# Kernel tuning notes

Hardware: AMD Instinct MI355X
Metric: run time of the kernel (lower is better)

## Reference

```python
import jax, jax.numpy as jnp
import numpy as np

N = 50000
E = 800000
HIDDEN = 128
NUM_HEADS = 8
D_HEAD = HIDDEN // NUM_HEADS


def setup_inputs() -> dict:
    key = jax.random.key(0)
    ks = jax.random.split(key, 12)
    sc = 1.0 / np.sqrt(HIDDEN)
    inp = {
        "h": jax.random.normal(ks[0], (N, HIDDEN), dtype=jnp.float32),
        "rows": jax.random.randint(ks[1], (E,), 0, N, dtype=jnp.int32),
        "cols": jax.random.randint(ks[2], (E,), 0, N, dtype=jnp.int32),
        "Wq": jax.random.normal(ks[3], (HIDDEN, HIDDEN), dtype=jnp.float32) * sc,
        "bq": jax.random.normal(ks[4], (HIDDEN,), dtype=jnp.float32) * sc,
        "Wk": jax.random.normal(ks[5], (HIDDEN, HIDDEN), dtype=jnp.float32) * sc,
        "bk": jax.random.normal(ks[6], (HIDDEN,), dtype=jnp.float32) * sc,
        "Wv": jax.random.normal(ks[7], (HIDDEN, HIDDEN), dtype=jnp.float32) * sc,
        "bv": jax.random.normal(ks[8], (HIDDEN,), dtype=jnp.float32) * sc,
        "Wo": jax.random.normal(ks[9], (HIDDEN, HIDDEN), dtype=jnp.float32) * sc,
        "bo": jax.random.normal(ks[10], (HIDDEN,), dtype=jnp.float32) * sc,
    }
    return inp


def reference(h, rows, cols, Wq, bq, Wk, bk, Wv, bv, Wo, bo):
    n = h.shape[0]
    scaling = D_HEAD ** (-0.5)
    # projections; torch-style reshape splits hidden as (d_head, num_heads)
    q = ((h @ Wq.T + bq).reshape(n, D_HEAD, NUM_HEADS)) * scaling
    k = (h @ Wk.T + bk).reshape(n, D_HEAD, NUM_HEADS)
    v = (h @ Wv.T + bv).reshape(n, D_HEAD, NUM_HEADS)
    # SDDMM: per-edge, per-head score = q[row] . k[col]   -> [E, H]
    scores = jnp.einsum("edh,edh->eh", q[rows], k[cols])
    # row-wise (destination) stable softmax over variable-degree neighborhoods
    m = jax.ops.segment_max(scores, rows, num_segments=n)  # [N, H]
    e = jnp.exp(scores - m[rows])
    s = jax.ops.segment_sum(e, rows, num_segments=n)  # [N, H]
    attn = e / s[rows]  # [E, H]
    # SpMM: out[i] = sum_{(i,j) in E} attn[e] * v[j]
    out = jax.ops.segment_sum(attn[:, None, :] * v[cols], rows, num_segments=n)
    return out.reshape(n, HIDDEN) @ Wo.T + bo
```

## Files before the change

### kernel.cpp

```cpp
#include <hip/hip_runtime.h>
#include <math.h>

#define N_NODES 50000
#define N_EDGES 800000
#define HID 128
#define CAP 64

#define SCAT_TH   (N_EDGES / 8)
#define SCAT_BLK  ((SCAT_TH + 255) / 256)
#define WCVT_BLK  64
#define HCVT_BLK  (N_NODES * HID / 4 / 256)
#define PREP_BLK  (SCAT_BLK + WCVT_BLK + HCVT_BLK)

#define QKV_BX    ((N_NODES + 31) / 32)
#define ATTN_BLK  ((N_NODES + 3) / 4)
#define OUT_BLK   ((N_NODES + 63) / 64)

typedef _Float16 f16_t;
typedef f16_t f16x8 __attribute__((ext_vector_type(8)));
typedef f16_t f16x2 __attribute__((ext_vector_type(2)));
typedef float f32x4 __attribute__((ext_vector_type(4)));

__device__ __forceinline__ ushort f2h_bits(float x) {
    union { f16_t h; ushort u; } c; c.h = (f16_t)x; return c.u;
}
__device__ __forceinline__ f16x2 as_h2(uint u) {
    union { uint u_; f16x2 h; } c; c.u_ = u; return c.h;
}

__global__ __launch_bounds__(256) void prep(
    const float* __restrict__ h,
    const float* __restrict__ Wq, const float* __restrict__ Wk,
    const float* __restrict__ Wv, const float* __restrict__ Wo,
    ushort* __restrict__ hf, ushort* __restrict__ wf,
    const int* __restrict__ rows, const int* __restrict__ cols,
    int* __restrict__ cnt, ushort* __restrict__ slots)
{
    const int b = blockIdx.x;
    const int tid = threadIdx.x;

    if (b < SCAT_BLK) {
        const int t = b * 256 + tid;
        if (t < SCAT_TH) {
            const int4* r4 = (const int4*)rows + (size_t)t * 2;
            const int4* c4 = (const int4*)cols + (size_t)t * 2;
            int4 ra = r4[0], rb2 = r4[1];
            int4 ca = c4[0], cb = c4[1];
            const int r[8] = {ra.x, ra.y, ra.z, ra.w, rb2.x, rb2.y, rb2.z, rb2.w};
            const int c[8] = {ca.x, ca.y, ca.z, ca.w, cb.x, cb.y, cb.z, cb.w};
            int p[8];
#pragma unroll
            for (int u = 0; u < 8; ++u)
                p[u] = atomicAdd(&cnt[r[u] << 4], 1);
#pragma unroll
            for (int u = 0; u < 8; ++u)
                if (p[u] < CAP) slots[(size_t)r[u] * CAP + p[u]] = (ushort)c[u];
        }
    } else if (b < SCAT_BLK + WCVT_BLK) {
        const int t = (b - SCAT_BLK) * 256 + tid;
        const int m = t >> 12, i = t & 4095;
        const float* src = (m == 0) ? Wq : (m == 1) ? Wk : (m == 2) ? Wv : Wo;
        float4 f = ((const float4*)src)[i];
        ushort4 o;
        o.x = f2h_bits(f.x); o.y = f2h_bits(f.y);
        o.z = f2h_bits(f.z); o.w = f2h_bits(f.w);
        ((ushort4*)(wf + m * 16384))[i] = o;
    } else {
        const int t = (b - SCAT_BLK - WCVT_BLK) * 256 + tid;
        float4 f = ((const float4*)h)[t];
        ushort4 o;
        o.x = f2h_bits(f.x); o.y = f2h_bits(f.y);
        o.z = f2h_bits(f.z); o.w = f2h_bits(f.w);
        ((ushort4*)hf)[t] = o;
    }
}

__global__ __launch_bounds__(256) void gemm_qkv(
    const ushort* __restrict__ hf, const ushort* __restrict__ wf,
    const float* __restrict__ bq, const float* __restrict__ bk,
    const float* __restrict__ bv,
    uint* __restrict__ qp, uint2* __restrict__ kv)
{
    const int lane = threadIdx.x & 63;
    const int wid  = threadIdx.x >> 6;
    const int mrow = lane & 15;
    const int quad = lane >> 4;
    const int rb   = blockIdx.x * 32;
    const int T    = blockIdx.y * 4 + wid;
    const int c    = T * 16 + mrow;

    f16x8 a[2][4];
#pragma unroll
    for (int s = 0; s < 2; ++s) {
        int ar = rb + s * 16 + mrow;
        if (ar >= N_NODES) ar = N_NODES - 1;
        const ushort* ap = hf + (size_t)ar * HID + quad * 8;
#pragma unroll
        for (int kc = 0; kc < 4; ++kc) a[s][kc] = *(const f16x8*)(ap + kc * 32);
    }
    f16x8 bQ[4], bK[4], bV[4];
#pragma unroll
    for (int kc = 0; kc < 4; ++kc) {
        const int off = c * HID + kc * 32 + quad * 8;
        bQ[kc] = *(const f16x8*)(wf + off);
        bK[kc] = *(const f16x8*)(wf + 16384 + off);
        bV[kc] = *(const f16x8*)(wf + 32768 + off);
    }

    f32x4 aq[2], ak[2], av[2];
#pragma unroll
    for (int s = 0; s < 2; ++s) {
        aq[s] = (f32x4){0.f, 0.f, 0.f, 0.f};
        ak[s] = (f32x4){0.f, 0.f, 0.f, 0.f};
        av[s] = (f32x4){0.f, 0.f, 0.f, 0.f};
    }
#pragma unroll
    for (int s = 0; s < 2; ++s)
#pragma unroll
        for (int kc = 0; kc < 4; ++kc) {
            aq[s] = __builtin_amdgcn_mfma_f32_16x16x32_f16(a[s][kc], bQ[kc], aq[s], 0, 0, 0);
            ak[s] = __builtin_amdgcn_mfma_f32_16x16x32_f16(a[s][kc], bK[kc], ak[s], 0, 0, 0);
            av[s] = __builtin_amdgcn_mfma_f32_16x16x32_f16(a[s][kc], bV[kc], av[s], 0, 0, 0);
        }

    const float bqc = bq[c], bkc = bk[c], bvc = bv[c];
    const bool  lo  = (mrow & 8) == 0;
    const int   i   = mrow & 7;
#pragma unroll
    for (int s = 0; s < 2; ++s)
#pragma unroll
        for (int r = 0; r < 4; ++r) {
            const int orow = rb + s * 16 + quad * 4 + r;
            uint qv = f2h_bits((aq[s][r] + bqc) * 0.25f);
            uint kb = f2h_bits(ak[s][r] + bkc);
            uint vb = f2h_bits(av[s][r] + bvc);
            uint qh = __shfl_xor((int)qv, 8);
            uint kh = __shfl_xor((int)kb, 8);
            uint vh = __shfl_xor((int)vb, 8);
            if (lo && orow < N_NODES) {
                const size_t base = (size_t)orow * 64 + 8 * T + i;
                qp[base] = qv | (qh << 16);
                kv[base] = make_uint2(kb | (kh << 16), vb | (vh << 16));
            }
        }
}

__device__ __forceinline__ void edge_acc(uint2 rr, f16x2 qh,
                                         float& l, float& Oa, float& Ob)
{
    float p = __builtin_amdgcn_fdot2(as_h2(rr.x), qh, 0.f, false);
    p += __shfl_xor(p, 8);
    p += __shfl_xor(p, 16);
    p += __shfl_xor(p, 32);
    float ex = __expf(p);
    f16x2 vh = as_h2(rr.y);
    l  += ex;
    Oa += ex * (float)vh[0];
    Ob += ex * (float)vh[1];
}

__global__ __launch_bounds__(256) void attn(
    const uint* __restrict__ qp, const uint2* __restrict__ kv,
    const int* __restrict__ cnt, const ushort* __restrict__ slots,
    ushort* __restrict__ ao)
{
    const int lane = threadIdx.x & 63;
    const int node = blockIdx.x * 4 + (threadIdx.x >> 6);
    if (node >= N_NODES) return;

    const f16x2 qh = as_h2(qp[(size_t)node * 64 + lane]);

    int deg = cnt[node << 4];
    if (deg > CAP) deg = CAP;
    const int myslot = (lane < deg) ? (int)slots[(size_t)node * CAP + lane] : 0;

    float ls[4] = {0.f, 0.f, 0.f, 0.f};
    float Oa[4] = {0.f, 0.f, 0.f, 0.f};
    float Ob[4] = {0.f, 0.f, 0.f, 0.f};

    int j = 0;
    for (; j + 4 <= deg; j += 4) {
        int s0 = __shfl(myslot, j);
        int s1 = __shfl(myslot, j + 1);
        int s2 = __shfl(myslot, j + 2);
        int s3 = __shfl(myslot, j + 3);
        uint2 r0 = kv[(size_t)s0 * 64 + lane];
        uint2 r1 = kv[(size_t)s1 * 64 + lane];
        uint2 r2 = kv[(size_t)s2 * 64 + lane];
        uint2 r3 = kv[(size_t)s3 * 64 + lane];
        edge_acc(r0, qh, ls[0], Oa[0], Ob[0]);
        edge_acc(r1, qh, ls[1], Oa[1], Ob[1]);
        edge_acc(r2, qh, ls[2], Oa[2], Ob[2]);
        edge_acc(r3, qh, ls[3], Oa[3], Ob[3]);
    }
    for (; j < deg; ++j) {
        int s = __shfl(myslot, j);
        uint2 rr = kv[(size_t)s * 64 + lane];
        edge_acc(rr, qh, ls[0], Oa[0], Ob[0]);
    }

    const float l  = (ls[0] + ls[1]) + (ls[2] + ls[3]);
    const float O0 = (Oa[0] + Oa[1]) + (Oa[2] + Oa[3]);
    const float O1 = (Ob[0] + Ob[1]) + (Ob[2] + Ob[3]);
    const float inv = (l > 0.f) ? 1.f / l : 0.f;

    const int ce = 16 * (lane >> 3) + (lane & 7);
    ao[(size_t)node * HID + ce]     = f2h_bits(O0 * inv);
    ao[(size_t)node * HID + ce + 8] = f2h_bits(O1 * inv);
}

__global__ __launch_bounds__(256) void gemm_out(
    const ushort* __restrict__ A, const ushort* __restrict__ wfo,
    const float* __restrict__ bias, float* __restrict__ out)
{
    const int lane = threadIdx.x & 63;
    const int wid  = threadIdx.x >> 6;
    const int mrow = lane & 15;
    const int quad = lane >> 4;
    const int rb   = blockIdx.x * 64;

    const int c0 = wid * 32 + mrow;
    const int c1 = c0 + 16;

    f16x8 a[4][4];
#pragma unroll
    for (int s = 0; s < 4; ++s) {
        int ar = rb + s * 16 + mrow;
        if (ar >= N_NODES) ar = N_NODES - 1;
        const ushort* ap = A + (size_t)ar * HID + quad * 8;
#pragma unroll
        for (int kc = 0; kc < 4; ++kc) a[s][kc] = *(const f16x8*)(ap + kc * 32);
    }
    f16x8 b0[4], b1[4];
#pragma unroll
    for (int kc = 0; kc < 4; ++kc) {
        b0[kc] = *(const f16x8*)(wfo + c0 * HID + kc * 32 + quad * 8);
        b1[kc] = *(const f16x8*)(wfo + c1 * HID + kc * 32 + quad * 8);
    }

    f32x4 acc[4][2];
#pragma unroll
    for (int s = 0; s < 4; ++s) {
        acc[s][0] = (f32x4){0.f, 0.f, 0.f, 0.f};
        acc[s][1] = (f32x4){0.f, 0.f, 0.f, 0.f};
    }
#pragma unroll
    for (int s = 0; s < 4; ++s)
#pragma unroll
        for (int kc = 0; kc < 4; ++kc) {
            acc[s][0] = __builtin_amdgcn_mfma_f32_16x16x32_f16(a[s][kc], b0[kc], acc[s][0], 0, 0, 0);
            acc[s][1] = __builtin_amdgcn_mfma_f32_16x16x32_f16(a[s][kc], b1[kc], acc[s][1], 0, 0, 0);
        }

    const float bc0 = bias[c0], bc1 = bias[c1];
#pragma unroll
    for (int s = 0; s < 4; ++s)
#pragma unroll
        for (int r = 0; r < 4; ++r) {
            const int orow = rb + s * 16 + quad * 4 + r;
            if (orow < N_NODES) {
                out[(size_t)orow * HID + c0] = acc[s][0][r] + bc0;
                out[(size_t)orow * HID + c1] = acc[s][1][r] + bc1;
            }
        }
}

extern "C" void kernel_launch(void* const* d_in, const int* in_sizes, int n_in,
                              void* d_out, int out_size, void* d_ws, size_t ws_size,
                              hipStream_t stream)
{
    const float* h    = (const float*)d_in[0];
    const int*   rows = (const int*)  d_in[1];
    const int*   cols = (const int*)  d_in[2];
    const float* Wq   = (const float*)d_in[3];
    const float* bq   = (const float*)d_in[4];
    const float* Wk   = (const float*)d_in[5];
    const float* bk   = (const float*)d_in[6];
    const float* Wv   = (const float*)d_in[7];
    const float* bv   = (const float*)d_in[8];
    const float* Wo   = (const float*)d_in[9];
    const float* bo   = (const float*)d_in[10];
    float* out = (float*)d_out;

    char* ws = (char*)d_ws;
    uint*   qp    = (uint*)ws;    ws += (size_t)N_NODES * 64 * 4;
    uint2*  kv    = (uint2*)ws;   ws += (size_t)N_NODES * 64 * 8;
    ushort* hf    = (ushort*)ws;  ws += (size_t)N_NODES * HID * 2;
    ushort* ao    = (ushort*)ws;  ws += (size_t)N_NODES * HID * 2;
    ushort* wf    = (ushort*)ws;  ws += 4 * 16384 * 2;
    int*    cnt   = (int*)ws;     ws += (size_t)N_NODES * 64;
    ushort* slots = (ushort*)ws;

    hipMemsetAsync(cnt, 0, (size_t)N_NODES * 64, stream);

    dim3 blk(256);
    prep<<<PREP_BLK, blk, 0, stream>>>(h, Wq, Wk, Wv, Wo, hf, wf,
                                       rows, cols, cnt, slots);
    gemm_qkv<<<dim3(QKV_BX, 2), blk, 0, stream>>>(hf, wf, bq, bk, bv, qp, kv);
    attn<<<ATTN_BLK, blk, 0, stream>>>(qp, kv, cnt, slots, ao);
    gemm_out<<<OUT_BLK, blk, 0, stream>>>(ao, wf + 3 * 16384, bo, out);
}
```

Before: 234.6 us.

## Fuse edge scatter with QKV GEMM and convert h to fp16 in-register

```diff
diff --git a/kernel.cpp b/kernel.cpp
--- a/kernel.cpp
+++ b/kernel.cpp
@@ -8,13 +8,14 @@
 
 #define SCAT_TH   (N_EDGES / 8)
 #define SCAT_BLK  ((SCAT_TH + 255) / 256)
+#define QKV_BX    ((N_NODES + 31) / 32)
+#define FUSE_BLK  (SCAT_BLK + QKV_BX * 2)
+#define ATTN_BLK  ((N_NODES + 3) / 4)
+#define OUT_BLK   ((N_NODES + 31) / 32)
+
+#define ZERO_BLK  ((200000 + 255) / 256)
 #define WCVT_BLK  64
-#define HCVT_BLK  (N_NODES * HID / 4 / 256)
-#define PREP_BLK  (SCAT_BLK + WCVT_BLK + HCVT_BLK)
-
-#define QKV_BX    ((N_NODES + 31) / 32)
-#define ATTN_BLK  ((N_NODES + 3) / 4)
-#define OUT_BLK   ((N_NODES + 63) / 64)
+#define INIT_BLK  (ZERO_BLK + WCVT_BLK)
 
 typedef _Float16 f16_t;
 typedef f16_t f16x8 __attribute__((ext_vector_type(8)));
@@ -27,20 +28,46 @@
 __device__ __forceinline__ f16x2 as_h2(uint u) {
     union { uint u_; f16x2 h; } c; c.u_ = u; return c.h;
 }
-
-__global__ __launch_bounds__(256) void prep(
-    const float* __restrict__ h,
+__device__ __forceinline__ f16x8 cvt8(const float* p) {
+    float4 f0 = *(const float4*)p;
+    float4 f1 = *(const float4*)(p + 4);
+    f16x8 r;
+    r[0] = (f16_t)f0.x; r[1] = (f16_t)f0.y; r[2] = (f16_t)f0.z; r[3] = (f16_t)f0.w;
+    r[4] = (f16_t)f1.x; r[5] = (f16_t)f1.y; r[6] = (f16_t)f1.z; r[7] = (f16_t)f1.w;
+    return r;
+}
+
+__global__ __launch_bounds__(256) void init(
     const float* __restrict__ Wq, const float* __restrict__ Wk,
     const float* __restrict__ Wv, const float* __restrict__ Wo,
-    ushort* __restrict__ hf, ushort* __restrict__ wf,
+    ushort* __restrict__ wf, int* __restrict__ cnt)
+{
+    const int b = blockIdx.x;
+    if (b < ZERO_BLK) {
+        const int t = b * 256 + threadIdx.x;
+        if (t < 200000) ((int4*)cnt)[t] = make_int4(0, 0, 0, 0);
+    } else {
+        const int t = (b - ZERO_BLK) * 256 + threadIdx.x;
+        const int m = t >> 12, i = t & 4095;
+        const float* src = (m == 0) ? Wq : (m == 1) ? Wk : (m == 2) ? Wv : Wo;
+        float4 f = ((const float4*)src)[i];
+        ushort4 o;
+        o.x = f2h_bits(f.x); o.y = f2h_bits(f.y);
+        o.z = f2h_bits(f.z); o.w = f2h_bits(f.w);
+        ((ushort4*)(wf + m * 16384))[i] = o;
+    }
+}
+
+__global__ __launch_bounds__(256) void scatter_qkv(
+    const float* __restrict__ h, const ushort* __restrict__ wf,
+    const float* __restrict__ bq, const float* __restrict__ bk,
+    const float* __restrict__ bv,
     const int* __restrict__ rows, const int* __restrict__ cols,
-    int* __restrict__ cnt, ushort* __restrict__ slots)
-{
-    const int b = blockIdx.x;
-    const int tid = threadIdx.x;
-
-    if (b < SCAT_BLK) {
-        const int t = b * 256 + tid;
+    int* __restrict__ cnt, ushort* __restrict__ slots,
+    uint* __restrict__ qp, uint2* __restrict__ kv)
+{
+    if (blockIdx.x < SCAT_BLK) {
+        const int t = blockIdx.x * 256 + threadIdx.x;
         if (t < SCAT_TH) {
             const int4* r4 = (const int4*)rows + (size_t)t * 2;
             const int4* c4 = (const int4*)cols + (size_t)t * 2;
@@ -56,37 +83,16 @@
             for (int u = 0; u < 8; ++u)
                 if (p[u] < CAP) slots[(size_t)r[u] * CAP + p[u]] = (ushort)c[u];
         }
-    } else if (b < SCAT_BLK + WCVT_BLK) {
-        const int t = (b - SCAT_BLK) * 256 + tid;
-        const int m = t >> 12, i = t & 4095;
-        const float* src = (m == 0) ? Wq : (m == 1) ? Wk : (m == 2) ? Wv : Wo;
-        float4 f = ((const float4*)src)[i];
-        ushort4 o;
-        o.x = f2h_bits(f.x); o.y = f2h_bits(f.y);
-        o.z = f2h_bits(f.z); o.w = f2h_bits(f.w);
-        ((ushort4*)(wf + m * 16384))[i] = o;
-    } else {
-        const int t = (b - SCAT_BLK - WCVT_BLK) * 256 + tid;
-        float4 f = ((const float4*)h)[t];
-        ushort4 o;
-        o.x = f2h_bits(f.x); o.y = f2h_bits(f.y);
-        o.z = f2h_bits(f.z); o.w = f2h_bits(f.w);
-        ((ushort4*)hf)[t] = o;
-    }
-}
-
-__global__ __launch_bounds__(256) void gemm_qkv(
-    const ushort* __restrict__ hf, const ushort* __restrict__ wf,
-    const float* __restrict__ bq, const float* __restrict__ bk,
-    const float* __restrict__ bv,
-    uint* __restrict__ qp, uint2* __restrict__ kv)
-{
+        return;
+    }
+
+    const int b2   = blockIdx.x - SCAT_BLK;
     const int lane = threadIdx.x & 63;
     const int wid  = threadIdx.x >> 6;
     const int mrow = lane & 15;
     const int quad = lane >> 4;
-    const int rb   = blockIdx.x * 32;
-    const int T    = blockIdx.y * 4 + wid;
+    const int rb   = (b2 >> 1) * 32;
+    const int T    = (b2 & 1) * 4 + wid;
     const int c    = T * 16 + mrow;
 
     f16x8 a[2][4];
@@ -94,9 +100,9 @@
     for (int s = 0; s < 2; ++s) {
         int ar = rb + s * 16 + mrow;
         if (ar >= N_NODES) ar = N_NODES - 1;
-        const ushort* ap = hf + (size_t)ar * HID + quad * 8;
-#pragma unroll
-        for (int kc = 0; kc < 4; ++kc) a[s][kc] = *(const f16x8*)(ap + kc * 32);
+        const float* ap = h + (size_t)ar * HID + quad * 8;
+#pragma unroll
+        for (int kc = 0; kc < 4; ++kc) a[s][kc] = cvt8(ap + kc * 32);
     }
     f16x8 bQ[4], bK[4], bV[4];
 #pragma unroll
@@ -217,14 +223,14 @@
     const int wid  = threadIdx.x >> 6;
     const int mrow = lane & 15;
     const int quad = lane >> 4;
-    const int rb   = blockIdx.x * 64;
+    const int rb   = blockIdx.x * 32;
 
     const int c0 = wid * 32 + mrow;
     const int c1 = c0 + 16;
 
-    f16x8 a[4][4];
-#pragma unroll
-    for (int s = 0; s < 4; ++s) {
+    f16x8 a[2][4];
+#pragma unroll
+    for (int s = 0; s < 2; ++s) {
         int ar = rb + s * 16 + mrow;
         if (ar >= N_NODES) ar = N_NODES - 1;
         const ushort* ap = A + (size_t)ar * HID + quad * 8;
@@ -238,14 +244,14 @@
         b1[kc] = *(const f16x8*)(wfo + c1 * HID + kc * 32 + quad * 8);
     }
 
-    f32x4 acc[4][2];
-#pragma unroll
-    for (int s = 0; s < 4; ++s) {
+    f32x4 acc[2][2];
+#pragma unroll
+    for (int s = 0; s < 2; ++s) {
         acc[s][0] = (f32x4){0.f, 0.f, 0.f, 0.f};
         acc[s][1] = (f32x4){0.f, 0.f, 0.f, 0.f};
     }
 #pragma unroll
-    for (int s = 0; s < 4; ++s)
+    for (int s = 0; s < 2; ++s)
 #pragma unroll
         for (int kc = 0; kc < 4; ++kc) {
             acc[s][0] = __builtin_amdgcn_mfma_f32_16x16x32_f16(a[s][kc], b0[kc], acc[s][0], 0, 0, 0);
@@ -254,7 +260,7 @@
 
     const float bc0 = bias[c0], bc1 = bias[c1];
 #pragma unroll
-    for (int s = 0; s < 4; ++s)
+    for (int s = 0; s < 2; ++s)
 #pragma unroll
         for (int r = 0; r < 4; ++r) {
             const int orow = rb + s * 16 + quad * 4 + r;
@@ -285,18 +291,15 @@
     char* ws = (char*)d_ws;
     uint*   qp    = (uint*)ws;    ws += (size_t)N_NODES * 64 * 4;
     uint2*  kv    = (uint2*)ws;   ws += (size_t)N_NODES * 64 * 8;
-    ushort* hf    = (ushort*)ws;  ws += (size_t)N_NODES * HID * 2;
     ushort* ao    = (ushort*)ws;  ws += (size_t)N_NODES * HID * 2;
     ushort* wf    = (ushort*)ws;  ws += 4 * 16384 * 2;
     int*    cnt   = (int*)ws;     ws += (size_t)N_NODES * 64;
     ushort* slots = (ushort*)ws;
 
-    hipMemsetAsync(cnt, 0, (size_t)N_NODES * 64, stream);
-
     dim3 blk(256);
-    prep<<<PREP_BLK, blk, 0, stream>>>(h, Wq, Wk, Wv, Wo, hf, wf,
-                                       rows, cols, cnt, slots);
-    gemm_qkv<<<dim3(QKV_BX, 2), blk, 0, stream>>>(hf, wf, bq, bk, bv, qp, kv);
+    init<<<INIT_BLK, blk, 0, stream>>>(Wq, Wk, Wv, Wo, wf, cnt);
+    scatter_qkv<<<FUSE_BLK, blk, 0, stream>>>(h, wf, bq, bk, bv,
+                                              rows, cols, cnt, slots, qp, kv);
     attn<<<ATTN_BLK, blk, 0, stream>>>(qp, kv, cnt, slots, ao);
     gemm_out<<<OUT_BLK, blk, 0, stream>>>(ao, wf + 3 * 16384, bo, out);
 }
```

After: 234.7 us. Within noise of the previous version (+0.1%).
